# Optimization experiments

Hardware: AMD Instinct MI355X
Metric: run time of the kernel (lower is better)

## Reference

```python
import jax, jax.numpy as jnp
import numpy as np

NUM_GROUPS = 32
EPS = 1e-6


def setup_inputs() -> dict:
    key = jax.random.key(0)
    ks = jax.random.split(key, 4)
    B, C, H, W = 16, 512, 32, 32
    x = jax.random.normal(ks[0], (B, C, H, W), dtype=jnp.float32)
    norm_w = jnp.ones((C,), dtype=jnp.float32)
    norm_b = jnp.zeros((C,), dtype=jnp.float32)
    qkv_w = jax.random.normal(ks[1], (3 * C, C), dtype=jnp.float32) * (1.0 / np.sqrt(C))
    qkv_b = jnp.zeros((3 * C,), dtype=jnp.float32)
    proj_w = jax.random.normal(ks[2], (C, C), dtype=jnp.float32) * (1.0 / np.sqrt(C))
    proj_b = jnp.zeros((C,), dtype=jnp.float32)
    return {"x": x, "norm_w": norm_w, "norm_b": norm_b, "qkv_w": qkv_w,
            "qkv_b": qkv_b, "proj_w": proj_w, "proj_b": proj_b}


def _group_norm(x, w, b):
    B, C, H, W = x.shape
    g = NUM_GROUPS
    xg = x.reshape(B, g, C // g, H * W)
    mu = xg.mean(axis=(2, 3), keepdims=True)
    var = xg.var(axis=(2, 3), keepdims=True)
    xn = (xg - mu) * jax.lax.rsqrt(var + EPS)
    xn = xn.reshape(B, C, H, W)
    return xn * w[None, :, None, None] + b[None, :, None, None]


def reference(x, norm_w, norm_b, qkv_w, qkv_b, proj_w, proj_b):
    B, C, H, W = x.shape
    h = _group_norm(x, norm_w, norm_b)
    # 1x1 conv == channel GEMM
    qkv = jnp.einsum('oc,bchw->bohw', qkv_w, h) + qkv_b[None, :, None, None]
    q, k, v = jnp.split(qkv, 3, axis=1)
    N = H * W
    q = q.reshape(B, C, N)  # (b, c, n)
    k = k.reshape(B, C, N)
    v = v.reshape(B, C, N)
    scale = jnp.asarray(C, x.dtype) ** -0.5
    attn = jnp.einsum('bci,bcj->bij', q, k) * scale  # (b, Nq, Nk)
    attn = jax.nn.softmax(attn, axis=2)
    o = jnp.einsum('bcj,bij->bci', v, attn).reshape(B, C, H, W)
    out = jnp.einsum('oc,bchw->bohw', proj_w, o) + proj_b[None, :, None, None]
    return x + out
```

## Files before the change

kernel.cpp:

```cpp
#include <hip/hip_runtime.h>

typedef unsigned short u16;
typedef __bf16 bf16x8 __attribute__((ext_vector_type(8)));
typedef float f32x4 __attribute__((ext_vector_type(4)));

#define AS1 __attribute__((address_space(1)))
#define AS3 __attribute__((address_space(3)))


__device__ __forceinline__ u16 f2bf(float f) {
  union { float f; unsigned u; } v; v.f = f;
  return (u16)((v.u + 0x7fffu + ((v.u >> 16) & 1u)) >> 16);
}

__device__ __forceinline__ f32x4 mfma16(bf16x8 a, bf16x8 b, f32x4 c) {
  return __builtin_amdgcn_mfma_f32_16x16x32_bf16(a, b, c, 0, 0, 0);
}

__device__ __forceinline__ void stage_tile(const u16* __restrict__ src, size_t ld,
                                           u16* lds, int wv, int lane) {
#pragma unroll
  for (int h2 = 0; h2 < 2; h2++) {
    int rbase = wv * 32 + h2 * 16;
    int row = rbase + (lane >> 2);
    int segd = (lane & 3) ^ ((row >> 1) & 3);
    __builtin_amdgcn_global_load_lds(
        (const AS1 void*)(src + (size_t)row * ld + segd * 8),
        (AS3 void*)(lds + rbase * 32), 16, 0, 0);
  }
}

__device__ __forceinline__ bf16x8 ldsfrag(const u16* lds, int row, int rowq) {
  int q = rowq ^ ((row >> 1) & 3);
  return *(const bf16x8*)(lds + row * 32 + q * 8);
}

template<int NT>
__device__ __forceinline__ void gemm_core2(const u16* __restrict__ A, int lda,
                                           const u16* __restrict__ B, int ldb,
                                           u16* lds, f32x4 (&acc)[4][4],
                                           int wave, int lane) {
  u16* sA0 = lds;        u16* sA1 = lds + 4096;
  u16* sB0 = lds + 8192; u16* sB1 = lds + 12288;
  int wm = wave >> 1, wn = wave & 1;
  int col = lane & 15, rq = lane >> 4;
#pragma unroll
  for (int m = 0; m < 4; m++)
#pragma unroll
    for (int n = 0; n < 4; n++) acc[m][n] = (f32x4){0.f, 0.f, 0.f, 0.f};

  stage_tile(A, lda, sA0, wave, lane);
  stage_tile(B, ldb, sB0, wave, lane);
  stage_tile(A + 32, lda, sA1, wave, lane);
  stage_tile(B + 32, ldb, sB1, wave, lane);

  for (int t = 0; t < NT; t++) {
    u16* cA = (t & 1) ? sA1 : sA0;
    u16* cB = (t & 1) ? sB1 : sB0;
    if (t < NT - 1) {
      asm volatile("s_waitcnt vmcnt(4)" ::: "memory");
    } else {
      asm volatile("s_waitcnt vmcnt(0)" ::: "memory");
    }
    __builtin_amdgcn_sched_barrier(0);
    __builtin_amdgcn_s_barrier();
    __builtin_amdgcn_sched_barrier(0);
    bf16x8 af[4], bfr[4];
#pragma unroll
    for (int n = 0; n < 4; n++) bfr[n] = ldsfrag(cB, wn * 64 + n * 16 + col, rq);
#pragma unroll
    for (int m = 0; m < 4; m++) af[m] = ldsfrag(cA, wm * 64 + m * 16 + col, rq);
#pragma unroll
    for (int m = 0; m < 4; m++)
#pragma unroll
      for (int n = 0; n < 4; n++) acc[m][n] = mfma16(af[m], bfr[n], acc[m][n]);
    __builtin_amdgcn_sched_barrier(0);
    __builtin_amdgcn_s_barrier();
    if (t + 2 < NT) {
      stage_tile(A + (size_t)(t + 2) * 32, lda, cA, wave, lane);
      stage_tile(B + (size_t)(t + 2) * 32, ldb, cB, wave, lane);
    }
  }
}

__device__ __forceinline__ void epi_flush(const u16* lds, u16* gdst, size_t stride, int t) {
#pragma unroll
  for (int pass = 0; pass < 8; pass++) {
    int row = pass * 16 + (t >> 4);
    int ch = (t & 15) * 8;
    uint4 w = *(const uint4*)(lds + row * 132 + ch);
    *(uint4*)(gdst + (size_t)row * stride + ch) = w;
  }
}

__device__ __forceinline__ void stage_half(const u16* __restrict__ src, size_t ld,
                                           u16* ldsbase, int wave, int lane) {
#pragma unroll
  for (int r = 0; r < 2; r++) {
    int rb = (r * 8 + wave) * 8;
    int row = rb + (lane >> 3);
    int seg = (lane & 7) ^ (row & 7);
    __builtin_amdgcn_global_load_lds(
        (const AS1 void*)(src + (size_t)row * ld + seg * 8),
        (AS3 void*)(ldsbase + rb * 64), 16, 0, 0);
  }
}

template<int P>
__device__ __forceinline__ void phase_read(const u16* cA, const u16* cB,
                                           bf16x8 (&af)[2][2], bf16x8 (&bfr)[4][2],
                                           int wm, int wn, int col, int rq) {
  if constexpr (P == 0) {
#pragma unroll
    for (int nf = 0; nf < 4; nf++)
#pragma unroll
      for (int kk = 0; kk < 2; kk++) {
        int row = wn * 64 + nf * 16 + col;
        bfr[nf][kk] = *(const bf16x8*)(cB + row * 64 + (((kk << 2) + rq) ^ (row & 7)) * 8);
      }
  }
#pragma unroll
  for (int i = 0; i < 2; i++)
#pragma unroll
    for (int kk = 0; kk < 2; kk++) {
      int row = wm * 128 + (P * 2 + i) * 16 + col;
      af[i][kk] = *(const bf16x8*)(cA + row * 64 + (((kk << 2) + rq) ^ (row & 7)) * 8);
    }
}

template<int P>
__device__ __forceinline__ void phase_fma(const bf16x8 (&af)[2][2],
                                          const bf16x8 (&bfr)[4][2],
                                          f32x4 (&acc)[8][4]) {
#pragma unroll
  for (int i = 0; i < 2; i++)
#pragma unroll
    for (int kk = 0; kk < 2; kk++)
#pragma unroll
      for (int nf = 0; nf < 4; nf++)
        acc[P * 2 + i][nf] = mfma16(af[i][kk], bfr[nf][kk], acc[P * 2 + i][nf]);
}

#define RUN_PHASE(P, STAGE_CODE, WAIT_CODE)                                  \
  {                                                                          \
    bf16x8 af[2][2];                                                         \
    phase_read<P>(cA, cB, af, bfr, wm, wn, col, rq);                         \
    STAGE_CODE;                                                              \
    WAIT_CODE;                                                               \
    __builtin_amdgcn_sched_barrier(0);                                       \
    __builtin_amdgcn_s_barrier();                                            \
    __builtin_amdgcn_sched_barrier(0);                                       \
    __builtin_amdgcn_s_setprio(1);                                           \
    phase_fma<P>(af, bfr, acc);                                              \
    __builtin_amdgcn_s_setprio(0);                                           \
    __builtin_amdgcn_sched_barrier(0);                                       \
    __builtin_amdgcn_s_barrier();                                            \
    __builtin_amdgcn_sched_barrier(0);                                       \
  }

template<int NT>
__device__ __forceinline__ void gemm8_core(const u16* __restrict__ A, int lda,
                                           const u16* __restrict__ B, int ldb,
                                           u16* lds, f32x4 (&acc)[8][4],
                                           int wave, int lane) {
  u16* Abuf[2] = {lds, lds + 16384};
  u16* Bbuf[2] = {lds + 32768, lds + 49152};
  int wm = wave >> 2, wn = wave & 3;
  int col = lane & 15, rq = lane >> 4;
#pragma unroll
  for (int m = 0; m < 8; m++)
#pragma unroll
    for (int n = 0; n < 4; n++) acc[m][n] = (f32x4){0.f, 0.f, 0.f, 0.f};

  stage_half(A, lda, Abuf[0], wave, lane);
  stage_half(A + 128 * (size_t)lda, lda, Abuf[0] + 8192, wave, lane);
  stage_half(B, ldb, Bbuf[0], wave, lane);
  stage_half(B + 128 * (size_t)ldb, ldb, Bbuf[0] + 8192, wave, lane);
  stage_half(B + 64, ldb, Bbuf[1], wave, lane);
  stage_half(B + 64 + 128 * (size_t)ldb, ldb, Bbuf[1] + 8192, wave, lane);
  asm volatile("s_waitcnt vmcnt(4)" ::: "memory");
  __builtin_amdgcn_sched_barrier(0);
  __builtin_amdgcn_s_barrier();
  __builtin_amdgcn_sched_barrier(0);

  for (int kt = 0; kt < NT; kt++) {
    const u16* cA = Abuf[kt & 1];
    const u16* cB = Bbuf[kt & 1];
    u16* nA = Abuf[(kt + 1) & 1];
    u16* nB = Bbuf[kt & 1];
    const u16* Asrc = A + (size_t)(kt + 1) * 64;
    const u16* Bsrc = B + (size_t)(kt + 2) * 64;
    bool pa = (kt + 1 < NT), pb = (kt + 2 < NT);
    bf16x8 bfr[4][2];
    RUN_PHASE(0, if (pa) stage_half(Asrc, lda, nA, wave, lane), );
    RUN_PHASE(1, if (pa) stage_half(Asrc + 128 * (size_t)lda, lda, nA + 8192, wave, lane), );
    RUN_PHASE(2, if (pb) stage_half(Bsrc, ldb, nB, wave, lane), );
    RUN_PHASE(3, if (pb) stage_half(Bsrc + 128 * (size_t)ldb, ldb, nB + 8192, wave, lane),
              if (pb) { asm volatile("s_waitcnt vmcnt(4)" ::: "memory"); }
              else    { asm volatile("s_waitcnt vmcnt(0)" ::: "memory"); });
  }
}

__global__ __launch_bounds__(256) void gn_fused(const float* __restrict__ x,
                                                const float* __restrict__ gw,
                                                const float* __restrict__ gb,
                                                const float* __restrict__ qkv_w,
                                                const float* __restrict__ proj_w,
                                                u16* __restrict__ h,
                                                u16* __restrict__ wq,
                                                u16* __restrict__ wp) {
  __shared__ float buf[16 * 1032];
  __shared__ float ls[4], lss[4];
  int bg = blockIdx.x;
  int b = bg >> 5, g = bg & 31;
  const float4* p = (const float4*)(x + (size_t)bg * 16384);
  float s = 0.f, ss = 0.f;
  for (int i = threadIdx.x; i < 4096; i += 256) {
    float4 v = p[i];
    int c = i >> 8, n = (i & 255) * 4;
    *(float4*)&buf[c * 1032 + n] = v;
    s  += v.x + v.y + v.z + v.w;
    ss += v.x*v.x + v.y*v.y + v.z*v.z + v.w*v.w;
  }
  {
    int qb = bg * 384;
    for (int u = threadIdx.x; u < 384; u += 256) {
      float4 v = *(const float4*)(qkv_w + (size_t)(qb + u) * 4);
      int o = (qb + u) * 4;
      wq[o] = f2bf(v.x); wq[o+1] = f2bf(v.y); wq[o+2] = f2bf(v.z); wq[o+3] = f2bf(v.w);
    }
    int pb = bg * 128;
    if (threadIdx.x < 128) {
      float4 v = *(const float4*)(proj_w + (size_t)(pb + threadIdx.x) * 4);
      int o = (pb + threadIdx.x) * 4;
      wp[o] = f2bf(v.x); wp[o+1] = f2bf(v.y); wp[o+2] = f2bf(v.z); wp[o+3] = f2bf(v.w);
    }
  }
  for (int d = 32; d; d >>= 1) { s += __shfl_down(s, d); ss += __shfl_down(ss, d); }
  int wv = threadIdx.x >> 6;
  if ((threadIdx.x & 63) == 0) { ls[wv] = s; lss[wv] = ss; }
  __syncthreads();
  float m = (ls[0] + ls[1] + ls[2] + ls[3]) * (1.f / 16384.f);
  float var = (lss[0] + lss[1] + lss[2] + lss[3]) * (1.f / 16384.f) - m * m;
  float r = rsqrtf(var + 1e-6f);
  int c0 = g * 16;
  float w[16], bb[16];
#pragma unroll
  for (int c = 0; c < 16; c++) {
    w[c] = gw[c0 + c] * r;
    bb[c] = gb[c0 + c] - m * w[c];
  }
  for (int n = threadIdx.x; n < 1024; n += 256) {
    u16 o[16];
#pragma unroll
    for (int c = 0; c < 16; c++) o[c] = f2bf(buf[c * 1032 + n] * w[c] + bb[c]);
    u16* dst = h + (((size_t)((b << 10) | n)) << 9) + c0;
    *(uint4*)dst = *(uint4*)o;
    *(uint4*)(dst + 8) = *(uint4*)(o + 8);
  }
}

__global__ __launch_bounds__(256, 4) void gemm_qkv(const u16* __restrict__ A,
                                                   const u16* __restrict__ Bn,
                                                   const float* __restrict__ bias,
                                                   u16* __restrict__ q_nc,
                                                   u16* __restrict__ k_nc,
                                                   u16* __restrict__ v) {
  __shared__ u16 lds[16896];
  int bid = blockIdx.x;
  int xcd = bid & 7, r = bid >> 3;
  int mb = r % 12, nb = xcd * 16 + r / 12;
  int m0 = mb * 128, n0 = nb * 128;
  int t = threadIdx.x, wave = t >> 6, lane = t & 63;
  int wm = wave >> 1, wn = wave & 1;
  int col = lane & 15, rq = lane >> 4;
  f32x4 acc[4][4];
  gemm_core2<16>(A + (size_t)m0 * 512, 512, Bn + (size_t)n0 * 512, 512,
                 lds, acc, wave, lane);
  __syncthreads();
  if (mb < 8) {
#pragma unroll
    for (int i = 0; i < 4; i++)
#pragma unroll
      for (int j = 0; j < 4; j++) {
        int o = m0 + wm * 64 + i * 16 + rq * 4;
        u16 tmp[4];
#pragma unroll
        for (int rr = 0; rr < 4; rr++) tmp[rr] = f2bf(acc[i][j][rr] + bias[o + rr]);
        int bnl = wn * 64 + j * 16 + col;
        int chl = wm * 64 + i * 16 + rq * 4;
        *(uint2*)(lds + bnl * 132 + chl) = *(uint2*)tmp;
      }
    __syncthreads();
    u16* dst = ((mb < 4) ? q_nc : k_nc) + (size_t)n0 * 512 + (m0 & 511);
    epi_flush(lds, dst, 512, t);
  } else {
#pragma unroll
    for (int i = 0; i < 4; i++)
#pragma unroll
      for (int j = 0; j < 4; j++)
#pragma unroll
        for (int rr = 0; rr < 4; rr++) {
          int o = m0 + wm * 64 + i * 16 + rq * 4 + rr;
          int chl = wm * 64 + i * 16 + rq * 4 + rr;
          int bnl = wn * 64 + j * 16 + col;
          lds[chl * 132 + bnl] = f2bf(acc[i][j][rr] + bias[o]);
        }
    __syncthreads();
    u16* dst = v + (size_t)(m0 - 1024) * 16384 + n0;
    epi_flush(lds, dst, 16384, t);
  }
}

__global__ __launch_bounds__(512, 1) void gemm8_s(const u16* __restrict__ q_nc,
                                                  const u16* __restrict__ k_nc,
                                                  u16* __restrict__ E,
                                                  float* __restrict__ part) {
  __shared__ u16 lds[65536];
  int bid = blockIdx.x;
  int xcd = bid & 7, r = bid >> 3;
  int b = xcd * 2 + (r & 1);
  int tile = r >> 1;
  int m0 = (tile >> 2) * 256, n0 = (tile & 3) * 256;
  int t = threadIdx.x, wave = t >> 6, lane = t & 63;
  int wm = wave >> 2, wn = wave & 3;
  int col = lane & 15, rq = lane >> 4;
  f32x4 acc[8][4];
  gemm8_core<8>(q_nc + ((size_t)(b * 1024 + m0)) * 512, 512,
                k_nc + ((size_t)(b * 1024 + n0)) * 512, 512,
                lds, acc, wave, lane);
  float* pb = part + ((size_t)b << 14);
  int idx = (n0 >> 6) + wn;
  const float scale = 0.04419417382415922f;
  __syncthreads();
#pragma unroll
  for (int mf = 0; mf < 8; mf++)
#pragma unroll
    for (int rr = 0; rr < 4; rr++) {
      float e[4], rs = 0.f;
#pragma unroll
      for (int nf = 0; nf < 4; nf++) { e[nf] = __expf(acc[mf][nf][rr] * scale); rs += e[nf]; }
      rs += __shfl_xor(rs, 1); rs += __shfl_xor(rs, 2);
      rs += __shfl_xor(rs, 4); rs += __shfl_xor(rs, 8);
      int il = wm * 128 + mf * 16 + rq * 4 + rr;
      if (col == 0) pb[(m0 + il) * 16 + idx] = rs;
#pragma unroll
      for (int nf = 0; nf < 4; nf++) {
        int j = wn * 64 + nf * 16 + col;
        int jb = (j >> 3) ^ (il & 7);
        lds[il * 256 + (jb << 3) + (j & 7)] = f2bf(e[nf]);
      }
    }
  __syncthreads();
  u16* Eb = E + ((size_t)b << 20) + (size_t)m0 * 1024 + n0;
#pragma unroll
  for (int pass = 0; pass < 16; pass++) {
    int row = pass * 16 + (t >> 5);
    int jbl = t & 31;
    uint4 w = *(const uint4*)(lds + row * 256 + (jbl << 3));
    int jb = jbl ^ (row & 7);
    *(uint4*)(Eb + (size_t)row * 1024 + (jb << 3)) = w;
  }
}

__global__ __launch_bounds__(256, 4) void gemm_pv(const u16* __restrict__ E,
                                                  const u16* __restrict__ v,
                                                  const float* __restrict__ part,
                                                  u16* __restrict__ o_nc) {
  __shared__ u16 lds[16896];
  __shared__ float invs[128];
  int bid = blockIdx.x;
  int xcd = bid & 7, r = bid >> 3;
  int b = xcd * 2 + (r & 1);
  int tile = r >> 1;
  int m0 = (tile >> 2) * 128, n0 = (tile & 3) * 128;
  int t = threadIdx.x, wave = t >> 6, lane = t & 63;
  int wm = wave >> 1, wn = wave & 1;
  int col = lane & 15, rq = lane >> 4;
  f32x4 acc[4][4];
  gemm_core2<32>(E + ((size_t)b << 20) + (size_t)m0 * 1024, 1024,
                 v + (size_t)n0 * 16384 + ((size_t)b << 10), 16384,
                 lds, acc, wave, lane);
  if (t < 128) {
    const float4* p = (const float4*)(part + ((size_t)((b << 10) + m0 + t)) * 16);
    float4 a = p[0], bq = p[1], c = p[2], d = p[3];
    float s = a.x+a.y+a.z+a.w + bq.x+bq.y+bq.z+bq.w + c.x+c.y+c.z+c.w + d.x+d.y+d.z+d.w;
    invs[t] = 1.f / s;
  }
  __syncthreads();
#pragma unroll
  for (int i = 0; i < 4; i++)
#pragma unroll
    for (int rr = 0; rr < 4; rr++) {
      int iil = wm * 64 + i * 16 + rq * 4 + rr;
      float sc = invs[iil];
#pragma unroll
      for (int j = 0; j < 4; j++)
        lds[iil * 132 + wn * 64 + j * 16 + col] = f2bf(acc[i][j][rr] * sc);
    }
  __syncthreads();
  epi_flush(lds, o_nc + ((size_t)(b * 1024 + m0)) * 512 + n0, 512, t);
}

__global__ __launch_bounds__(256, 4) void gemm_proj(const u16* __restrict__ A,
                                                    const u16* __restrict__ Bn,
                                                    const float* __restrict__ bias,
                                                    const float* __restrict__ xres,
                                                    float* __restrict__ outp) {
  __shared__ u16 lds[16384];
  int bid = blockIdx.x;
  int xcd = bid & 7, r = bid >> 3;
  int mb = r & 3, nb = xcd * 16 + (r >> 2);
  int m0 = mb * 128, n0 = nb * 128;
  int t = threadIdx.x, wave = t >> 6, lane = t & 63;
  int wm = wave >> 1, wn = wave & 1;
  int col = lane & 15, rq = lane >> 4;
  f32x4 acc[4][4];
  gemm_core2<16>(A + (size_t)m0 * 512, 512, Bn + (size_t)n0 * 512, 512,
                 lds, acc, wave, lane);
#pragma unroll
  for (int i = 0; i < 4; i++)
#pragma unroll
    for (int j = 0; j < 4; j++)
#pragma unroll
      for (int rr = 0; rr < 4; rr++) {
        int co = m0 + wm * 64 + i * 16 + rq * 4 + rr;
        int bn = n0 + wn * 64 + j * 16 + col;
        int bb = bn >> 10, n = bn & 1023;
        size_t oi = (((size_t)(bb * 512 + co)) << 10) + n;
        outp[oi] = acc[i][j][rr] + bias[co] + xres[oi];
      }
}

extern "C" void kernel_launch(void* const* d_in, const int* in_sizes, int n_in,
                              void* d_out, int out_size, void* d_ws, size_t ws_size,
                              hipStream_t stream) {
  const float* x      = (const float*)d_in[0];
  const float* norm_w = (const float*)d_in[1];
  const float* norm_b = (const float*)d_in[2];
  const float* qkv_w  = (const float*)d_in[3];
  const float* qkv_b  = (const float*)d_in[4];
  const float* proj_w = (const float*)d_in[5];
  const float* proj_b = (const float*)d_in[6];
  float* out = (float*)d_out;

  char* ws = (char*)d_ws;
  size_t off = 0;
  auto alloc = [&](size_t bytes) {
    void* p = ws + off;
    off += (bytes + 255) & ~(size_t)255;
    return p;
  };
  float* part = (float*)alloc((size_t)16384 * 16 * 4);
  u16* wq   = (u16*)alloc((size_t)1536 * 512 * 2);
  u16* wp   = (u16*)alloc((size_t)512 * 512 * 2);
  u16* h    = (u16*)alloc((size_t)16384 * 512 * 2);
  u16* q_nc = (u16*)alloc((size_t)16384 * 512 * 2);
  u16* k_nc = (u16*)alloc((size_t)16384 * 512 * 2);
  u16* v    = (u16*)alloc((size_t)512 * 16384 * 2);
  u16* E    = (u16*)alloc((size_t)16 * 1024 * 1024 * 2);
  u16* o_nc = h;
  (void)in_sizes; (void)n_in; (void)out_size; (void)ws_size;

  gn_fused<<<512, 256, 0, stream>>>(x, norm_w, norm_b, qkv_w, proj_w, h, wq, wp);
  gemm_qkv<<<1536, 256, 0, stream>>>(wq, h, qkv_b, q_nc, k_nc, v);
  gemm8_s<<<256, 512, 0, stream>>>(q_nc, k_nc, E, part);
  gemm_pv<<<512, 256, 0, stream>>>(E, v, part, o_nc);
  gemm_proj<<<512, 256, 0, stream>>>(wp, o_nc, proj_b, x, out);
}
```

Baseline: 132.3 us.

## Triple-buffer GEMM LDS staging to drop the second barrier per K-step

```diff
diff --git a/kernel.cpp b/kernel.cpp
--- a/kernel.cpp
+++ b/kernel.cpp
@@ -36,12 +36,12 @@
 }
 
 template<int NT>
-__device__ __forceinline__ void gemm_core2(const u16* __restrict__ A, int lda,
+__device__ __forceinline__ void gemm_core3(const u16* __restrict__ A, int lda,
                                            const u16* __restrict__ B, int ldb,
                                            u16* lds, f32x4 (&acc)[4][4],
                                            int wave, int lane) {
-  u16* sA0 = lds;        u16* sA1 = lds + 4096;
-  u16* sB0 = lds + 8192; u16* sB1 = lds + 12288;
+  u16* a0 = lds;         u16* a1 = lds + 4096;  u16* a2 = lds + 8192;
+  u16* b0 = lds + 12288; u16* b1 = lds + 16384; u16* b2 = lds + 20480;
   int wm = wave >> 1, wn = wave & 1;
   int col = lane & 15, rq = lane >> 4;
 #pragma unroll
@@ -49,14 +49,12 @@
 #pragma unroll
     for (int n = 0; n < 4; n++) acc[m][n] = (f32x4){0.f, 0.f, 0.f, 0.f};
 
-  stage_tile(A, lda, sA0, wave, lane);
-  stage_tile(B, ldb, sB0, wave, lane);
-  stage_tile(A + 32, lda, sA1, wave, lane);
-  stage_tile(B + 32, ldb, sB1, wave, lane);
+  stage_tile(A, lda, a0, wave, lane);
+  stage_tile(B, ldb, b0, wave, lane);
+  stage_tile(A + 32, lda, a1, wave, lane);
+  stage_tile(B + 32, ldb, b1, wave, lane);
 
   for (int t = 0; t < NT; t++) {
-    u16* cA = (t & 1) ? sA1 : sA0;
-    u16* cB = (t & 1) ? sB1 : sB0;
     if (t < NT - 1) {
       asm volatile("s_waitcnt vmcnt(4)" ::: "memory");
     } else {
@@ -65,21 +63,21 @@
     __builtin_amdgcn_sched_barrier(0);
     __builtin_amdgcn_s_barrier();
     __builtin_amdgcn_sched_barrier(0);
+    if (t + 2 < NT) {
+      stage_tile(A + (size_t)(t + 2) * 32, lda, a2, wave, lane);
+      stage_tile(B + (size_t)(t + 2) * 32, ldb, b2, wave, lane);
+    }
     bf16x8 af[4], bfr[4];
 #pragma unroll
-    for (int n = 0; n < 4; n++) bfr[n] = ldsfrag(cB, wn * 64 + n * 16 + col, rq);
-#pragma unroll
-    for (int m = 0; m < 4; m++) af[m] = ldsfrag(cA, wm * 64 + m * 16 + col, rq);
+    for (int n = 0; n < 4; n++) bfr[n] = ldsfrag(b0, wn * 64 + n * 16 + col, rq);
+#pragma unroll
+    for (int m = 0; m < 4; m++) af[m] = ldsfrag(a0, wm * 64 + m * 16 + col, rq);
 #pragma unroll
     for (int m = 0; m < 4; m++)
 #pragma unroll
       for (int n = 0; n < 4; n++) acc[m][n] = mfma16(af[m], bfr[n], acc[m][n]);
-    __builtin_amdgcn_sched_barrier(0);
-    __builtin_amdgcn_s_barrier();
-    if (t + 2 < NT) {
-      stage_tile(A + (size_t)(t + 2) * 32, lda, cA, wave, lane);
-      stage_tile(B + (size_t)(t + 2) * 32, ldb, cB, wave, lane);
-    }
+    u16* ta = a0; a0 = a1; a1 = a2; a2 = ta;
+    u16* tb = b0; b0 = b1; b1 = b2; b2 = tb;
   }
 }
 
@@ -260,13 +258,13 @@
   }
 }
 
-__global__ __launch_bounds__(256, 4) void gemm_qkv(const u16* __restrict__ A,
+__global__ __launch_bounds__(256, 3) void gemm_qkv(const u16* __restrict__ A,
                                                    const u16* __restrict__ Bn,
                                                    const float* __restrict__ bias,
                                                    u16* __restrict__ q_nc,
                                                    u16* __restrict__ k_nc,
                                                    u16* __restrict__ v) {
-  __shared__ u16 lds[16896];
+  __shared__ u16 lds[24576];
   int bid = blockIdx.x;
   int xcd = bid & 7, r = bid >> 3;
   int mb = r % 12, nb = xcd * 16 + r / 12;
@@ -275,7 +273,7 @@
   int wm = wave >> 1, wn = wave & 1;
   int col = lane & 15, rq = lane >> 4;
   f32x4 acc[4][4];
-  gemm_core2<16>(A + (size_t)m0 * 512, 512, Bn + (size_t)n0 * 512, 512,
+  gemm_core3<16>(A + (size_t)m0 * 512, 512, Bn + (size_t)n0 * 512, 512,
                  lds, acc, wave, lane);
   __syncthreads();
   if (mb < 8) {
@@ -363,11 +361,11 @@
   }
 }
 
-__global__ __launch_bounds__(256, 4) void gemm_pv(const u16* __restrict__ E,
+__global__ __launch_bounds__(256, 3) void gemm_pv(const u16* __restrict__ E,
                                                   const u16* __restrict__ v,
                                                   const float* __restrict__ part,
                                                   u16* __restrict__ o_nc) {
-  __shared__ u16 lds[16896];
+  __shared__ u16 lds[24576];
   __shared__ float invs[128];
   int bid = blockIdx.x;
   int xcd = bid & 7, r = bid >> 3;
@@ -378,7 +376,7 @@
   int wm = wave >> 1, wn = wave & 1;
   int col = lane & 15, rq = lane >> 4;
   f32x4 acc[4][4];
-  gemm_core2<32>(E + ((size_t)b << 20) + (size_t)m0 * 1024, 1024,
+  gemm_core3<32>(E + ((size_t)b << 20) + (size_t)m0 * 1024, 1024,
                  v + (size_t)n0 * 16384 + ((size_t)b << 10), 16384,
                  lds, acc, wave, lane);
   if (t < 128) {
@@ -402,12 +400,12 @@
   epi_flush(lds, o_nc + ((size_t)(b * 1024 + m0)) * 512 + n0, 512, t);
 }
 
-__global__ __launch_bounds__(256, 4) void gemm_proj(const u16* __restrict__ A,
+__global__ __launch_bounds__(256, 3) void gemm_proj(const u16* __restrict__ A,
                                                     const u16* __restrict__ Bn,
                                                     const float* __restrict__ bias,
                                                     const float* __restrict__ xres,
                                                     float* __restrict__ outp) {
-  __shared__ u16 lds[16384];
+  __shared__ u16 lds[24576];
   int bid = blockIdx.x;
   int xcd = bid & 7, r = bid >> 3;
   int mb = r & 3, nb = xcd * 16 + (r >> 2);
@@ -416,7 +414,7 @@
   int wm = wave >> 1, wn = wave & 1;
   int col = lane & 15, rq = lane >> 4;
   f32x4 acc[4][4];
-  gemm_core2<16>(A + (size_t)m0 * 512, 512, Bn + (size_t)n0 * 512, 512,
+  gemm_core3<16>(A + (size_t)m0 * 512, 512, Bn + (size_t)n0 * 512, 512,
                  lds, acc, wave, lane);
 #pragma unroll
   for (int i = 0; i < 4; i++)
```

After: 133.5 us, median of 3. No clear change (+0.9%).

## Widen GEMM tiles to 128x256 with 8-wave blocks for qkv, pv, proj

Applied to the files above, without the earlier changes.

```diff
diff --git a/kernel.cpp b/kernel.cpp
--- a/kernel.cpp
+++ b/kernel.cpp
@@ -30,35 +30,44 @@
   }
 }
 
+__device__ __forceinline__ void stage_a128(const u16* __restrict__ src, size_t ld,
+                                           u16* lds, int wv, int lane) {
+  int row = wv * 16 + (lane >> 2);
+  int segd = (lane & 3) ^ ((row >> 1) & 3);
+  __builtin_amdgcn_global_load_lds(
+      (const AS1 void*)(src + (size_t)row * ld + segd * 8),
+      (AS3 void*)(lds + wv * 512), 16, 0, 0);
+}
+
 __device__ __forceinline__ bf16x8 ldsfrag(const u16* lds, int row, int rowq) {
   int q = rowq ^ ((row >> 1) & 3);
   return *(const bf16x8*)(lds + row * 32 + q * 8);
 }
 
 template<int NT>
-__device__ __forceinline__ void gemm_core2(const u16* __restrict__ A, int lda,
-                                           const u16* __restrict__ B, int ldb,
-                                           u16* lds, f32x4 (&acc)[4][4],
-                                           int wave, int lane) {
-  u16* sA0 = lds;        u16* sA1 = lds + 4096;
-  u16* sB0 = lds + 8192; u16* sB1 = lds + 12288;
-  int wm = wave >> 1, wn = wave & 1;
+__device__ __forceinline__ void gemm_hw(const u16* __restrict__ A, int lda,
+                                        const u16* __restrict__ B, int ldb,
+                                        u16* lds, f32x4 (&acc)[4][4],
+                                        int wave, int lane) {
+  u16* sA0 = lds;          u16* sA1 = lds + 4096;
+  u16* sB0 = lds + 8192;   u16* sB1 = lds + 16384;
+  int wm = wave >> 2, wn = wave & 3;
   int col = lane & 15, rq = lane >> 4;
 #pragma unroll
   for (int m = 0; m < 4; m++)
 #pragma unroll
     for (int n = 0; n < 4; n++) acc[m][n] = (f32x4){0.f, 0.f, 0.f, 0.f};
 
-  stage_tile(A, lda, sA0, wave, lane);
+  stage_a128(A, lda, sA0, wave, lane);
   stage_tile(B, ldb, sB0, wave, lane);
-  stage_tile(A + 32, lda, sA1, wave, lane);
+  stage_a128(A + 32, lda, sA1, wave, lane);
   stage_tile(B + 32, ldb, sB1, wave, lane);
 
   for (int t = 0; t < NT; t++) {
     u16* cA = (t & 1) ? sA1 : sA0;
     u16* cB = (t & 1) ? sB1 : sB0;
     if (t < NT - 1) {
-      asm volatile("s_waitcnt vmcnt(4)" ::: "memory");
+      asm volatile("s_waitcnt vmcnt(3)" ::: "memory");
     } else {
       asm volatile("s_waitcnt vmcnt(0)" ::: "memory");
     }
@@ -77,16 +86,16 @@
     __builtin_amdgcn_sched_barrier(0);
     __builtin_amdgcn_s_barrier();
     if (t + 2 < NT) {
-      stage_tile(A + (size_t)(t + 2) * 32, lda, cA, wave, lane);
+      stage_a128(A + (size_t)(t + 2) * 32, lda, cA, wave, lane);
       stage_tile(B + (size_t)(t + 2) * 32, ldb, cB, wave, lane);
     }
   }
 }
 
-__device__ __forceinline__ void epi_flush(const u16* lds, u16* gdst, size_t stride, int t) {
-#pragma unroll
-  for (int pass = 0; pass < 8; pass++) {
-    int row = pass * 16 + (t >> 4);
+__device__ __forceinline__ void epi_flush512(const u16* lds, u16* gdst, size_t stride, int t) {
+#pragma unroll
+  for (int pass = 0; pass < 4; pass++) {
+    int row = pass * 32 + (t >> 4);
     int ch = (t & 15) * 8;
     uint4 w = *(const uint4*)(lds + row * 132 + ch);
     *(uint4*)(gdst + (size_t)row * stride + ch) = w;
@@ -260,55 +269,66 @@
   }
 }
 
-__global__ __launch_bounds__(256, 4) void gemm_qkv(const u16* __restrict__ A,
+__global__ __launch_bounds__(512, 4) void gemm_qkv(const u16* __restrict__ A,
                                                    const u16* __restrict__ Bn,
                                                    const float* __restrict__ bias,
                                                    u16* __restrict__ q_nc,
                                                    u16* __restrict__ k_nc,
                                                    u16* __restrict__ v) {
-  __shared__ u16 lds[16896];
+  __shared__ u16 lds[24576];
   int bid = blockIdx.x;
   int xcd = bid & 7, r = bid >> 3;
-  int mb = r % 12, nb = xcd * 16 + r / 12;
-  int m0 = mb * 128, n0 = nb * 128;
+  int mb = r % 12, nb = xcd * 8 + r / 12;
+  int m0 = mb * 128, n0 = nb * 256;
   int t = threadIdx.x, wave = t >> 6, lane = t & 63;
-  int wm = wave >> 1, wn = wave & 1;
+  int wm = wave >> 2, wn = wave & 3;
   int col = lane & 15, rq = lane >> 4;
   f32x4 acc[4][4];
-  gemm_core2<16>(A + (size_t)m0 * 512, 512, Bn + (size_t)n0 * 512, 512,
-                 lds, acc, wave, lane);
-  __syncthreads();
+  gemm_hw<16>(A + (size_t)m0 * 512, 512, Bn + (size_t)n0 * 512, 512,
+              lds, acc, wave, lane);
   if (mb < 8) {
-#pragma unroll
-    for (int i = 0; i < 4; i++)
-#pragma unroll
-      for (int j = 0; j < 4; j++) {
-        int o = m0 + wm * 64 + i * 16 + rq * 4;
-        u16 tmp[4];
-#pragma unroll
-        for (int rr = 0; rr < 4; rr++) tmp[rr] = f2bf(acc[i][j][rr] + bias[o + rr]);
-        int bnl = wn * 64 + j * 16 + col;
-        int chl = wm * 64 + i * 16 + rq * 4;
-        *(uint2*)(lds + bnl * 132 + chl) = *(uint2*)tmp;
+    u16* dst = ((mb < 4) ? q_nc : k_nc) + (size_t)n0 * 512 + (m0 & 511);
+#pragma unroll
+    for (int h = 0; h < 2; h++) {
+      __syncthreads();
+      if ((wn >> 1) == h) {
+#pragma unroll
+        for (int i = 0; i < 4; i++)
+#pragma unroll
+          for (int j = 0; j < 4; j++) {
+            int o = m0 + wm * 64 + i * 16 + rq * 4;
+            u16 tmp[4];
+#pragma unroll
+            for (int rr = 0; rr < 4; rr++) tmp[rr] = f2bf(acc[i][j][rr] + bias[o + rr]);
+            int bnl = (wn & 1) * 64 + j * 16 + col;
+            int chl = wm * 64 + i * 16 + rq * 4;
+            *(uint2*)(lds + bnl * 132 + chl) = *(uint2*)tmp;
+          }
       }
-    __syncthreads();
-    u16* dst = ((mb < 4) ? q_nc : k_nc) + (size_t)n0 * 512 + (m0 & 511);
-    epi_flush(lds, dst, 512, t);
+      __syncthreads();
+      epi_flush512(lds, dst + (size_t)(h * 128) * 512, 512, t);
+    }
   } else {
-#pragma unroll
-    for (int i = 0; i < 4; i++)
-#pragma unroll
-      for (int j = 0; j < 4; j++)
-#pragma unroll
-        for (int rr = 0; rr < 4; rr++) {
-          int o = m0 + wm * 64 + i * 16 + rq * 4 + rr;
-          int chl = wm * 64 + i * 16 + rq * 4 + rr;
-          int bnl = wn * 64 + j * 16 + col;
-          lds[chl * 132 + bnl] = f2bf(acc[i][j][rr] + bias[o]);
-        }
-    __syncthreads();
     u16* dst = v + (size_t)(m0 - 1024) * 16384 + n0;
-    epi_flush(lds, dst, 16384, t);
+#pragma unroll
+    for (int h = 0; h < 2; h++) {
+      __syncthreads();
+      if ((wn >> 1) == h) {
+#pragma unroll
+        for (int i = 0; i < 4; i++)
+#pragma unroll
+          for (int j = 0; j < 4; j++)
+#pragma unroll
+            for (int rr = 0; rr < 4; rr++) {
+              int o = m0 + wm * 64 + i * 16 + rq * 4 + rr;
+              int chl = wm * 64 + i * 16 + rq * 4 + rr;
+              int bnl = (wn & 1) * 64 + j * 16 + col;
+              lds[chl * 132 + bnl] = f2bf(acc[i][j][rr] + bias[o]);
+            }
+      }
+      __syncthreads();
+      epi_flush512(lds, dst + h * 128, 16384, t);
+    }
   }
 }
 
@@ -363,24 +383,24 @@
   }
 }
 
-__global__ __launch_bounds__(256, 4) void gemm_pv(const u16* __restrict__ E,
+__global__ __launch_bounds__(512, 4) void gemm_pv(const u16* __restrict__ E,
                                                   const u16* __restrict__ v,
                                                   const float* __restrict__ part,
                                                   u16* __restrict__ o_nc) {
-  __shared__ u16 lds[16896];
+  __shared__ u16 lds[24576];
   __shared__ float invs[128];
   int bid = blockIdx.x;
   int xcd = bid & 7, r = bid >> 3;
   int b = xcd * 2 + (r & 1);
   int tile = r >> 1;
-  int m0 = (tile >> 2) * 128, n0 = (tile & 3) * 128;
+  int m0 = (tile >> 1) * 128, n0 = (tile & 1) * 256;
   int t = threadIdx.x, wave = t >> 6, lane = t & 63;
-  int wm = wave >> 1, wn = wave & 1;
+  int wm = wave >> 2, wn = wave & 3;
   int col = lane & 15, rq = lane >> 4;
   f32x4 acc[4][4];
-  gemm_core2<32>(E + ((size_t)b << 20) + (size_t)m0 * 1024, 1024,
-                 v + (size_t)n0 * 16384 + ((size_t)b << 10), 16384,
-                 lds, acc, wave, lane);
+  gemm_hw<32>(E + ((size_t)b << 20) + (size_t)m0 * 1024, 1024,
+              v + (size_t)n0 * 16384 + ((size_t)b << 10), 16384,
+              lds, acc, wave, lane);
   if (t < 128) {
     const float4* p = (const float4*)(part + ((size_t)((b << 10) + m0 + t)) * 16);
     float4 a = p[0], bq = p[1], c = p[2], d = p[3];
@@ -389,35 +409,43 @@
   }
   __syncthreads();
 #pragma unroll
-  for (int i = 0; i < 4; i++)
-#pragma unroll
-    for (int rr = 0; rr < 4; rr++) {
-      int iil = wm * 64 + i * 16 + rq * 4 + rr;
-      float sc = invs[iil];
-#pragma unroll
-      for (int j = 0; j < 4; j++)
-        lds[iil * 132 + wn * 64 + j * 16 + col] = f2bf(acc[i][j][rr] * sc);
-    }
-  __syncthreads();
-  epi_flush(lds, o_nc + ((size_t)(b * 1024 + m0)) * 512 + n0, 512, t);
-}
-
-__global__ __launch_bounds__(256, 4) void gemm_proj(const u16* __restrict__ A,
+  for (int h = 0; h < 2; h++) {
+    if (h) __syncthreads();
+    if ((wn >> 1) == h) {
+#pragma unroll
+      for (int i = 0; i < 4; i++)
+#pragma unroll
+        for (int rr = 0; rr < 4; rr++) {
+          int iil = wm * 64 + i * 16 + rq * 4 + rr;
+          float sc = invs[iil];
+#pragma unroll
+          for (int j = 0; j < 4; j++) {
+            int cl = (wn & 1) * 64 + j * 16 + col;
+            lds[iil * 132 + cl] = f2bf(acc[i][j][rr] * sc);
+          }
+        }
+    }
+    __syncthreads();
+    epi_flush512(lds, o_nc + ((size_t)(b * 1024 + m0)) * 512 + n0 + h * 128, 512, t);
+  }
+}
+
+__global__ __launch_bounds__(512, 4) void gemm_proj(const u16* __restrict__ A,
                                                     const u16* __restrict__ Bn,
                                                     const float* __restrict__ bias,
                                                     const float* __restrict__ xres,
                                                     float* __restrict__ outp) {
-  __shared__ u16 lds[16384];
+  __shared__ u16 lds[24576];
   int bid = blockIdx.x;
   int xcd = bid & 7, r = bid >> 3;
-  int mb = r & 3, nb = xcd * 16 + (r >> 2);
-  int m0 = mb * 128, n0 = nb * 128;
+  int mb = r & 3, nb = xcd * 8 + (r >> 2);
+  int m0 = mb * 128, n0 = nb * 256;
   int t = threadIdx.x, wave = t >> 6, lane = t & 63;
-  int wm = wave >> 1, wn = wave & 1;
+  int wm = wave >> 2, wn = wave & 3;
   int col = lane & 15, rq = lane >> 4;
   f32x4 acc[4][4];
-  gemm_core2<16>(A + (size_t)m0 * 512, 512, Bn + (size_t)n0 * 512, 512,
-                 lds, acc, wave, lane);
+  gemm_hw<16>(A + (size_t)m0 * 512, 512, Bn + (size_t)n0 * 512, 512,
+              lds, acc, wave, lane);
 #pragma unroll
   for (int i = 0; i < 4; i++)
 #pragma unroll
@@ -463,8 +491,8 @@
   (void)in_sizes; (void)n_in; (void)out_size; (void)ws_size;
 
   gn_fused<<<512, 256, 0, stream>>>(x, norm_w, norm_b, qkv_w, proj_w, h, wq, wp);
-  gemm_qkv<<<1536, 256, 0, stream>>>(wq, h, qkv_b, q_nc, k_nc, v);
+  gemm_qkv<<<768, 512, 0, stream>>>(wq, h, qkv_b, q_nc, k_nc, v);
   gemm8_s<<<256, 512, 0, stream>>>(q_nc, k_nc, E, part);
-  gemm_pv<<<512, 256, 0, stream>>>(E, v, part, o_nc);
-  gemm_proj<<<512, 256, 0, stream>>>(wp, o_nc, proj_b, x, out);
-}
+  gemm_pv<<<256, 512, 0, stream>>>(E, v, part, o_nc);
+  gemm_proj<<<256, 512, 0, stream>>>(wp, o_nc, proj_b, x, out);
+}
```

Result: no change. 134.4 us (+1.5%).
